# Kernel optimization log

Hardware: AMD Instinct MI355X
Metric: run time of the kernel (lower is better)

Reference implementation:

```python
import jax, jax.numpy as jnp
import numpy as np

NUM_HEADS = 8
STRIDE = 1
PAD = 1


def _conv(x, w, stride=STRIDE, pad=PAD):
    return jax.lax.conv_general_dilated(
        x, w, (stride, stride), [(pad, pad), (pad, pad)],
        dimension_numbers=("NCHW", "OIHW", "NCHW"))


def setup_inputs() -> dict:
    key = jax.random.key(0)
    ks = jax.random.split(key, 5)
    B, C, H, W = 8, 64, 56, 56
    nh = NUM_HEADS
    x = jax.random.normal(ks[0], (B, C, H, W), dtype=jnp.float32)
    # Conv weights, small init for numerical stability
    Wq = jax.random.normal(ks[1], (C * nh, C, 3, 3), dtype=jnp.float32) * 0.05
    Wk = jax.random.normal(ks[2], (C * nh, C, 3, 3), dtype=jnp.float32) * 0.05
    Wv = jax.random.normal(ks[3], (C * nh, C, 3, 3), dtype=jnp.float32) * 0.05
    Wu = jax.random.normal(ks[4], (C, C * nh, 1, 1), dtype=jnp.float32) * 0.05
    return {"x": x, "Wq": Wq, "Wk": Wk, "Wv": Wv, "Wu": Wu}


def reference(x, Wq, Wk, Wv, Wu):
    B, C, H, W = x.shape
    nh = NUM_HEADS
    # projections: [B, nh*C, H, W] -> [B, nh, C, H, W] -> [B, C, nh, H, W]
    def proj(w):
        y = _conv(x, w).reshape(B, nh, C, H, W)
        return jnp.transpose(y, (0, 2, 1, 3, 4))
    q = proj(Wq)  # [B, C, nh, H, W]
    k = proj(Wk)
    v = proj(Wv)
    scale = 1.0 / np.sqrt(C * nh).astype(np.float32)
    # contract over heads axis ('n'), attend over channel axis: [B, Cq, H, W, Ck]
    scores = jnp.einsum("bqnhw,bknhw->bqhwk", q, k) * scale
    attn = jax.nn.softmax(scores, axis=-1)
    # attended: [B, Cq, nh, H, W]
    attended = jnp.einsum("bqhwk,bknhw->bqnhw", attn, v)
    out = _conv(attended.reshape(B, C * nh, H, W), Wu, stride=1, pad=0)
    return jax.nn.relu(out)
```

## Files before the change

### kernel.cpp

```cpp
#include <hip/hip_runtime.h>
#include <hip/hip_bf16.h>

#define HW   56
#define CIN  64
#define OC   512
#define NPIX (HW * HW)
#define PEL  ((size_t)8 * NPIX * OC)

typedef unsigned short ushort_t;
typedef __attribute__((ext_vector_type(8))) short short8;
typedef __attribute__((ext_vector_type(4))) float floatx4;
typedef __attribute__((ext_vector_type(16))) float floatx16;

static __device__ __forceinline__ ushort_t f2bf(float f) {
  __hip_bfloat16 h = __float2bfloat16(f);
  return *(ushort_t*)&h;
}

__global__ __launch_bounds__(256)
void prep_kernel(const float* __restrict__ x, const float* __restrict__ W0,
                 const float* __restrict__ W1, const float* __restrict__ W2,
                 const float* __restrict__ Wu, ushort_t* __restrict__ xT,
                 ushort_t* __restrict__ Wb, ushort_t* __restrict__ WuP) {
  __shared__ ushort_t lx[CIN * HW];
  const int bid = blockIdx.x;
  const int tid = threadIdx.x;

  if (bid < 448) {
    const int h = bid % HW, b = bid / HW;
    for (int idx = tid; idx < CIN * HW; idx += 256) {
      int c = idx / HW, w = idx - c * HW;
      lx[idx] = f2bf(x[((size_t)(b * CIN + c) * HW + h) * HW + w]);
    }
    __syncthreads();
    ushort_t* dst = xT + ((size_t)(b * HW + h)) * HW * CIN;
    for (int i = tid; i < (CIN * HW) / 4; i += 256) {
      int e0 = i * 4;
      int w = e0 >> 6, c0 = e0 & 63;
      ushort4 o;
      o.x = lx[(c0 + 0) * HW + w];
      o.y = lx[(c0 + 1) * HW + w];
      o.z = lx[(c0 + 2) * HW + w];
      o.w = lx[(c0 + 3) * HW + w];
      ((ushort4*)dst)[i] = o;
    }
  } else if (bid < 832) {
    const int u = bid - 448;
    const int sel = u / 128;
    const int j = (u % 128) * 4 + (tid >> 6);
    const int cin = tid & 63;
    const float* W = sel == 0 ? W0 : (sel == 1 ? W1 : W2);
    ushort_t* Ds = Wb + (size_t)sel * 9 * OC * CIN;
    const int src = (sel < 2) ? ((j & 7) * 64 + (j >> 3)) : j;
    #pragma unroll
    for (int tap = 0; tap < 9; ++tap)
      Ds[((size_t)tap * OC + j) * CIN + cin] = f2bf(W[(size_t)src * 576 + cin * 9 + tap]);
  } else {
    const int el = (bid - 832) * 256 + tid;
    WuP[el] = f2bf(Wu[el]);
  }
}

#define XLS 72
#define XROW (58 * XLS)

__global__ __launch_bounds__(256, 2)
void conv3x3_qkv(const ushort_t* __restrict__ xT, const ushort_t* __restrict__ Wb,
                 ushort_t* __restrict__ yq) {
  __shared__ __align__(16) ushort_t xl[6 * XROW];

  const int tid  = threadIdx.x;
  const int lane = tid & 63;
  const int wv   = tid >> 6;
  const int g    = blockIdx.x;
  const int ob   = blockIdx.y;
  const int b    = blockIdx.z & 7;
  const int s    = blockIdx.z >> 3;
  const int h0   = g * 4;
  const int l31  = lane & 31;
  const int khi  = lane >> 5;

  int abase[7];
  #pragma unroll
  for (int t = 0; t < 7; ++t) {
    int p = t * 32 + l31;
    int row = p / HW, ww = p - row * HW;
    abase[t] = (row * 58 + ww) * XLS + khi * 8;
  }

  const ushort_t* wb0 = Wb + (size_t)s * 9 * OC * CIN +
                        ((size_t)(ob * 128 + wv * 32 + l31)) * CIN + khi * 8;

  for (int r = 0; r < 6; ++r) {
    int gh = h0 - 1 + r;
    if (gh >= 0 && gh < HW) {
      const uint4* src = (const uint4*)(xT + ((size_t)(b * HW + gh) * HW) * CIN);
      for (int idx = tid; idx < 448; idx += 256) {
        int w = idx >> 3, co = (idx & 7) * 8;
        *(uint4*)&xl[(r * 58 + 1 + w) * XLS + co] = src[idx];
      }
      if (tid < 16) {
        int col = (tid >> 3) ? 57 : 0, co = (tid & 7) * 8;
        *(uint4*)&xl[(r * 58 + col) * XLS + co] = (uint4){0, 0, 0, 0};
      }
    } else {
      for (int idx = tid; idx < 464; idx += 256) {
        int w = idx >> 3, co = (idx & 7) * 8;
        *(uint4*)&xl[(r * 58 + w) * XLS + co] = (uint4){0, 0, 0, 0};
      }
    }
  }

  short8 Bf[2][4];
  #pragma unroll
  for (int ck = 0; ck < 4; ++ck)
    Bf[0][ck] = *(const short8*)(wb0 + ck * 16);

  floatx16 acc[7];
  #pragma unroll
  for (int t = 0; t < 7; ++t) acc[t] = (floatx16)(0.0f);

  __syncthreads();

  #pragma unroll
  for (int tap = 0; tap < 9; ++tap) {
    const int p = tap & 1;
    if (tap < 8) {
      #pragma unroll
      for (int ck = 0; ck < 4; ++ck)
        Bf[p ^ 1][ck] = *(const short8*)(wb0 + (size_t)(tap + 1) * OC * CIN + ck * 16);
    }
    const int kh = tap / 3, kw = tap - kh * 3;
    #pragma unroll
    for (int ck = 0; ck < 4; ++ck) {
      #pragma unroll
      for (int t = 0; t < 7; ++t) {
        short8 af = *(const short8*)&xl[abase[t] + (kh * 58 + kw) * XLS + ck * 16];
        acc[t] = __builtin_amdgcn_mfma_f32_32x32x16_bf16(af, Bf[p][ck], acc[t], 0, 0, 0);
      }
    }
  }

  ushort_t* y = yq + (size_t)s * PEL;
  const int oc = ob * 128 + wv * 32 + l31;
  #pragma unroll
  for (int t = 0; t < 7; ++t) {
    #pragma unroll
    for (int i = 0; i < 16; ++i) {
      int p = t * 32 + (i & 3) + 8 * (i >> 2) + 4 * khi;
      int row = p / HW, ww = p - row * HW;
      size_t pb = ((size_t)((b * HW + h0 + row) * HW + ww)) * OC;
      y[pb + oc] = f2bf(acc[t][i]);
    }
  }
}

#define PST  72
#define A2ST 520

__global__ __launch_bounds__(256, 2)
void attn_kernel(const ushort_t* __restrict__ q, const ushort_t* __restrict__ k,
                 const ushort_t* __restrict__ v, const ushort_t* __restrict__ WuP,
                 float* __restrict__ out) {
  __shared__ __align__(16) ushort_t Pl[4][64 * PST];
  __shared__ __align__(16) ushort_t a2[16 * A2ST];

  const int tid  = threadIdx.x;
  const int lane = tid & 63;
  const int wv   = tid >> 6;
  const int l15  = lane & 15;
  const int quad = lane >> 4;
  const int p0   = blockIdx.x * 16;
  const int b    = blockIdx.y;
  const size_t ibase = ((size_t)b * NPIX + p0) * 512;

  ushort_t* Pw = &Pl[wv][0];
  const float scale = 0.044194173824159216f;

  auto loadpix = [&](int plocal, short8 qf[4], short8 kf[4], short8 vf[2]) {
    const ushort_t* qp = q + ibase + (size_t)plocal * 512;
    const ushort_t* kp = k + ibase + (size_t)plocal * 512;
    const ushort_t* vp = v + ibase + (size_t)plocal * 512;
    #pragma unroll
    for (int nt = 0; nt < 4; ++nt)
      qf[nt] = *(const short8*)(qp + (nt * 16 + l15) * 8);
    #pragma unroll
    for (int mt = 0; mt < 4; ++mt) {
      kf[mt] = (short8){0, 0, 0, 0, 0, 0, 0, 0};
      if (quad == 0) kf[mt] = *(const short8*)(kp + (mt * 16 + l15) * 8);
    }
    #pragma unroll
    for (int ck = 0; ck < 2; ++ck)
      vf[ck] = *(const short8*)(vp + (l15 & 7) * 64 + ck * 32 + quad * 8);
  };

  short8 qf[4], kf[4], vf[2];
  loadpix(wv * 4, qf, kf, vf);

  #pragma unroll
  for (int i = 0; i < 4; ++i) {
    const int plocal = wv * 4 + i;
    short8 qn[4], kn[4], vn[2];
    if (i < 3) loadpix(plocal + 1, qn, kn, vn);

    floatx4 S[4][4];
    #pragma unroll
    for (int mt = 0; mt < 4; ++mt)
      #pragma unroll
      for (int nt = 0; nt < 4; ++nt) S[mt][nt] = (floatx4){0.f, 0.f, 0.f, 0.f};
    #pragma unroll
    for (int mt = 0; mt < 4; ++mt)
      #pragma unroll
      for (int nt = 0; nt < 4; ++nt)
        S[mt][nt] = __builtin_amdgcn_mfma_f32_16x16x32_bf16(kf[mt], qf[nt], S[mt][nt], 0, 0, 0);

    #pragma unroll
    for (int nt = 0; nt < 4; ++nt) {
      float m = S[0][nt][0];
      #pragma unroll
      for (int mt = 0; mt < 4; ++mt)
        #pragma unroll
        for (int r = 0; r < 4; ++r) m = fmaxf(m, S[mt][nt][r]);
      m = fmaxf(m, __shfl_xor(m, 16));
      m = fmaxf(m, __shfl_xor(m, 32));
      float sum = 0.f;
      #pragma unroll
      for (int mt = 0; mt < 4; ++mt)
        #pragma unroll
        for (int r = 0; r < 4; ++r) {
          float e = __expf((S[mt][nt][r] - m) * scale);
          S[mt][nt][r] = e;
          sum += e;
        }
      sum += __shfl_xor(sum, 16);
      sum += __shfl_xor(sum, 32);
      float inv = __builtin_amdgcn_rcpf(sum);
      #pragma unroll
      for (int mt = 0; mt < 4; ++mt) {
        ushort4 w4;
        w4.x = f2bf(S[mt][nt][0] * inv);
        w4.y = f2bf(S[mt][nt][1] * inv);
        w4.z = f2bf(S[mt][nt][2] * inv);
        w4.w = f2bf(S[mt][nt][3] * inv);
        *(ushort4*)&Pw[(nt * 16 + l15) * PST + mt * 16 + quad * 4] = w4;
      }
    }

    floatx4 T[4];
    #pragma unroll
    for (int nt = 0; nt < 4; ++nt) T[nt] = (floatx4){0.f, 0.f, 0.f, 0.f};
    #pragma unroll
    for (int ck = 0; ck < 2; ++ck) {
      #pragma unroll
      for (int nt = 0; nt < 4; ++nt) {
        short8 pf = *(const short8*)&Pw[(nt * 16 + l15) * PST + ck * 32 + quad * 8];
        T[nt] = __builtin_amdgcn_mfma_f32_16x16x32_bf16(vf[ck], pf, T[nt], 0, 0, 0);
      }
    }
    if (quad < 2) {
      #pragma unroll
      for (int nt = 0; nt < 4; ++nt) {
        ushort4 w4;
        w4.x = f2bf(T[nt][0]);
        w4.y = f2bf(T[nt][1]);
        w4.z = f2bf(T[nt][2]);
        w4.w = f2bf(T[nt][3]);
        *(ushort4*)&a2[plocal * A2ST + (nt * 16 + l15) * 8 + quad * 4] = w4;
      }
    }

    if (i < 3) {
      #pragma unroll
      for (int z = 0; z < 4; ++z) { qf[z] = qn[z]; kf[z] = kn[z]; }
      vf[0] = vn[0];
      vf[1] = vn[1];
    }
  }
  __syncthreads();

  floatx4 O = (floatx4){0.f, 0.f, 0.f, 0.f};
  #pragma unroll
  for (int ck = 0; ck < 16; ++ck) {
    short8 aw = *(const short8*)(WuP + (size_t)(wv * 16 + l15) * 512 + ck * 32 + quad * 8);
    short8 bw = *(const short8*)&a2[l15 * A2ST + ck * 32 + quad * 8];
    O = __builtin_amdgcn_mfma_f32_16x16x32_bf16(aw, bw, O, 0, 0, 0);
  }
  #pragma unroll
  for (int r = 0; r < 4; ++r) {
    int co = wv * 16 + quad * 4 + r;
    out[((size_t)b * 64 + co) * NPIX + p0 + l15] = fmaxf(O[r], 0.f);
  }
}

extern "C" void kernel_launch(void* const* d_in, const int* in_sizes, int n_in,
                              void* d_out, int out_size, void* d_ws, size_t ws_size,
                              hipStream_t stream) {
  const float* x  = (const float*)d_in[0];
  const float* Wq = (const float*)d_in[1];
  const float* Wk = (const float*)d_in[2];
  const float* Wv = (const float*)d_in[3];
  const float* Wu = (const float*)d_in[4];
  float* out = (float*)d_out;

  const size_t xT_elems = (size_t)8 * NPIX * CIN;
  const size_t w_elems  = (size_t)9 * OC * CIN;
  const size_t wu_elems = (size_t)64 * 512;
  ushort_t* xT  = (ushort_t*)d_ws;
  ushort_t* Wb  = xT + xT_elems;
  ushort_t* WuP = Wb + 3 * w_elems;
  ushort_t* q   = WuP + wu_elems;
  ushort_t* k   = q + PEL;
  ushort_t* v   = k + PEL;

  prep_kernel<<<960, 256, 0, stream>>>(x, Wq, Wk, Wv, Wu, xT, Wb, WuP);

  dim3 cgrid(14, 4, 24);
  conv3x3_qkv<<<cgrid, 256, 0, stream>>>(xT, Wb, q);

  attn_kernel<<<dim3(NPIX / 16, 8), 256, 0, stream>>>(q, k, v, WuP, out);
}
```

Baseline: 175.3 us.

## Retile QKV conv to 2D warp grid with 512-thread blocks

The 3x3 conv kernel moves to 512-thread blocks of 8 warps arranged as 2 (pixel) x 4 (channel) groups. Each warp computes 4 pixel tiles of 28 rows by 2 output-channel tiles of 32, so every A fragment read from LDS feeds two MFMAs and each block covers 256 output channels. This halves the grid along the channel axis and halves how often the input halo is staged into LDS. The cost is padded 32-row MFMA tiles holding only 28 valid pixels, which wastes some MFMA work. The attention kernel's launch bounds also change to ask for 3 blocks per CU, which may limit its registers.

```diff
diff --git a/kernel.cpp b/kernel.cpp
--- a/kernel.cpp
+++ b/kernel.cpp
@@ -64,7 +64,7 @@
 #define XLS 72
 #define XROW (58 * XLS)
 
-__global__ __launch_bounds__(256, 2)
+__global__ __launch_bounds__(512, 2)
 void conv3x3_qkv(const ushort_t* __restrict__ xT, const ushort_t* __restrict__ Wb,
                  ushort_t* __restrict__ yq) {
   __shared__ __align__(16) ushort_t xl[6 * XROW];
@@ -72,6 +72,8 @@
   const int tid  = threadIdx.x;
   const int lane = tid & 63;
   const int wv   = tid >> 6;
+  const int wm   = wv >> 2;
+  const int wn   = wv & 3;
   const int g    = blockIdx.x;
   const int ob   = blockIdx.y;
   const int b    = blockIdx.z & 7;
@@ -80,22 +82,23 @@
   const int l31  = lane & 31;
   const int khi  = lane >> 5;
 
-  int abase[7];
-  #pragma unroll
-  for (int t = 0; t < 7; ++t) {
-    int p = t * 32 + l31;
+  int abase[4];
+  #pragma unroll
+  for (int mt = 0; mt < 4; ++mt) {
+    int p = (wm * 4 + mt) * 28 + l31;
+    p = p > 223 ? 223 : p;
     int row = p / HW, ww = p - row * HW;
-    abase[t] = (row * 58 + ww) * XLS + khi * 8;
+    abase[mt] = (row * 58 + ww) * XLS + khi * 8;
   }
 
   const ushort_t* wb0 = Wb + (size_t)s * 9 * OC * CIN +
-                        ((size_t)(ob * 128 + wv * 32 + l31)) * CIN + khi * 8;
+                        ((size_t)(ob * 256 + wn * 64 + l31)) * CIN + khi * 8;
 
   for (int r = 0; r < 6; ++r) {
     int gh = h0 - 1 + r;
     if (gh >= 0 && gh < HW) {
       const uint4* src = (const uint4*)(xT + ((size_t)(b * HW + gh) * HW) * CIN);
-      for (int idx = tid; idx < 448; idx += 256) {
+      for (int idx = tid; idx < 448; idx += 512) {
         int w = idx >> 3, co = (idx & 7) * 8;
         *(uint4*)&xl[(r * 58 + 1 + w) * XLS + co] = src[idx];
       }
@@ -104,21 +107,25 @@
         *(uint4*)&xl[(r * 58 + col) * XLS + co] = (uint4){0, 0, 0, 0};
       }
     } else {
-      for (int idx = tid; idx < 464; idx += 256) {
-        int w = idx >> 3, co = (idx & 7) * 8;
-        *(uint4*)&xl[(r * 58 + w) * XLS + co] = (uint4){0, 0, 0, 0};
-      }
-    }
-  }
-
-  short8 Bf[2][4];
+      for (int idx = tid; idx < 464; idx += 512) {
+        int col = idx >> 3, co = (idx & 7) * 8;
+        *(uint4*)&xl[(r * 58 + col) * XLS + co] = (uint4){0, 0, 0, 0};
+      }
+    }
+  }
+
+  short8 Bf[2][4][2];
   #pragma unroll
   for (int ck = 0; ck < 4; ++ck)
-    Bf[0][ck] = *(const short8*)(wb0 + ck * 16);
-
-  floatx16 acc[7];
-  #pragma unroll
-  for (int t = 0; t < 7; ++t) acc[t] = (floatx16)(0.0f);
+    #pragma unroll
+    for (int nt = 0; nt < 2; ++nt)
+      Bf[0][ck][nt] = *(const short8*)(wb0 + (size_t)(nt * 32) * CIN + ck * 16);
+
+  floatx16 acc[4][2];
+  #pragma unroll
+  for (int mt = 0; mt < 4; ++mt)
+    #pragma unroll
+    for (int nt = 0; nt < 2; ++nt) acc[mt][nt] = (floatx16)(0.0f);
 
   __syncthreads();
 
@@ -128,29 +135,40 @@
     if (tap < 8) {
       #pragma unroll
       for (int ck = 0; ck < 4; ++ck)
-        Bf[p ^ 1][ck] = *(const short8*)(wb0 + (size_t)(tap + 1) * OC * CIN + ck * 16);
+        #pragma unroll
+        for (int nt = 0; nt < 2; ++nt)
+          Bf[p ^ 1][ck][nt] = *(const short8*)(wb0 + (size_t)(tap + 1) * OC * CIN +
+                                               (size_t)(nt * 32) * CIN + ck * 16);
     }
     const int kh = tap / 3, kw = tap - kh * 3;
+    const int toff = (kh * 58 + kw) * XLS;
     #pragma unroll
     for (int ck = 0; ck < 4; ++ck) {
       #pragma unroll
-      for (int t = 0; t < 7; ++t) {
-        short8 af = *(const short8*)&xl[abase[t] + (kh * 58 + kw) * XLS + ck * 16];
-        acc[t] = __builtin_amdgcn_mfma_f32_32x32x16_bf16(af, Bf[p][ck], acc[t], 0, 0, 0);
+      for (int mt = 0; mt < 4; ++mt) {
+        short8 af = *(const short8*)&xl[abase[mt] + toff + ck * 16];
+        acc[mt][0] = __builtin_amdgcn_mfma_f32_32x32x16_bf16(af, Bf[p][ck][0], acc[mt][0], 0, 0, 0);
+        acc[mt][1] = __builtin_amdgcn_mfma_f32_32x32x16_bf16(af, Bf[p][ck][1], acc[mt][1], 0, 0, 0);
       }
     }
   }
 
   ushort_t* y = yq + (size_t)s * PEL;
-  const int oc = ob * 128 + wv * 32 + l31;
-  #pragma unroll
-  for (int t = 0; t < 7; ++t) {
+  #pragma unroll
+  for (int mt = 0; mt < 4; ++mt) {
+    const int gm = wm * 4 + mt;
     #pragma unroll
     for (int i = 0; i < 16; ++i) {
-      int p = t * 32 + (i & 3) + 8 * (i >> 2) + 4 * khi;
+      int rl = (i & 3) + 8 * (i >> 2) + 4 * khi;
+      if (rl >= 28) continue;
+      int p = gm * 28 + rl;
       int row = p / HW, ww = p - row * HW;
       size_t pb = ((size_t)((b * HW + h0 + row) * HW + ww)) * OC;
-      y[pb + oc] = f2bf(acc[t][i]);
+      #pragma unroll
+      for (int nt = 0; nt < 2; ++nt) {
+        int oc = ob * 256 + wn * 64 + nt * 32 + l31;
+        y[pb + oc] = f2bf(acc[mt][nt][i]);
+      }
     }
   }
 }
@@ -158,7 +176,7 @@
 #define PST  72
 #define A2ST 520
 
-__global__ __launch_bounds__(256, 2)
+__global__ __launch_bounds__(256, 3)
 void attn_kernel(const ushort_t* __restrict__ q, const ushort_t* __restrict__ k,
                  const ushort_t* __restrict__ v, const ushort_t* __restrict__ WuP,
                  float* __restrict__ out) {
@@ -314,8 +332,8 @@
 
   prep_kernel<<<960, 256, 0, stream>>>(x, Wq, Wk, Wv, Wu, xT, Wb, WuP);
 
-  dim3 cgrid(14, 4, 24);
-  conv3x3_qkv<<<cgrid, 256, 0, stream>>>(xT, Wb, q);
+  dim3 cgrid(14, 2, 24);
+  conv3x3_qkv<<<cgrid, 512, 0, stream>>>(xT, Wb, q);
 
   attn_kernel<<<dim3(NPIX / 16, 8), 256, 0, stream>>>(q, k, v, WuP, out);
 }
```

New measurement: 182.3 us. 1.04x slower.
